# Kernel tuning notes

Measured on AMD Instinct MI355X. Metric: run time of the kernel, lower is better.

Reference implementation:

```python
import jax, jax.numpy as jnp
import numpy as np

D_MODEL = 1024
H = 16
D_K = D_MODEL // H
NEG = -1e9


def setup_inputs() -> dict:
    key = jax.random.key(0)
    ks = jax.random.split(key, 13)
    B, S = 4, 2048
    q = jax.random.normal(ks[0], (B, S, D_MODEL), dtype=jnp.float32)
    k = jax.random.normal(ks[1], (B, S, D_MODEL), dtype=jnp.float32)
    v = jax.random.normal(ks[2], (B, S, D_MODEL), dtype=jnp.float32)
    mask = jax.random.randint(ks[3], (B, 1, S, S), 0, 2, dtype=jnp.int32)
    s = 1.0 / np.sqrt(D_MODEL)
    wq = jax.random.uniform(ks[4], (D_MODEL, D_MODEL), jnp.float32, -s, s)
    bq = jax.random.uniform(ks[5], (D_MODEL,), jnp.float32, -s, s)
    wk = jax.random.uniform(ks[6], (D_MODEL, D_MODEL), jnp.float32, -s, s)
    bk = jax.random.uniform(ks[7], (D_MODEL,), jnp.float32, -s, s)
    wv = jax.random.uniform(ks[8], (D_MODEL, D_MODEL), jnp.float32, -s, s)
    bv = jax.random.uniform(ks[9], (D_MODEL,), jnp.float32, -s, s)
    wo = jax.random.uniform(ks[10], (D_MODEL, D_MODEL), jnp.float32, -s, s)
    bo = jax.random.uniform(ks[11], (D_MODEL,), jnp.float32, -s, s)
    return {"q": q, "k": k, "v": v, "mask": mask,
            "wq": wq, "bq": bq, "wk": wk, "bk": bk,
            "wv": wv, "bv": bv, "wo": wo, "bo": bo}


def reference(q, k, v, mask, wq, bq, wk, bk, wv, bv, wo, bo):
    B, S, _ = q.shape
    # projections (torch Linear: x @ W.T + b)
    query = q @ wq.T + bq
    key_ = k @ wk.T + bk
    value = v @ wv.T + bv
    # [B, S, H, D_K] -> [B, H, S, D_K]
    query = query.reshape(B, S, H, D_K).transpose(0, 2, 1, 3)
    key_ = key_.reshape(B, S, H, D_K).transpose(0, 2, 1, 3)
    value = value.reshape(B, S, H, D_K).transpose(0, 2, 1, 3)
    scores = jnp.einsum('bhqd,bhkd->bhqk', query, key_) / jnp.sqrt(jnp.float32(D_K))
    scores = jnp.where(mask == 0, jnp.float32(NEG), scores)
    attn = jax.nn.softmax(scores, axis=-1)  # dropout p=0 -> identity
    x = jnp.einsum('bhqk,bhkd->bhqd', attn, value)
    x = x.transpose(0, 2, 1, 3).reshape(B, S, D_MODEL)
    return x @ wo.T + bo
```

## Files before the change

### kernel.cpp

```cpp
#include <hip/hip_runtime.h>
#include <stdint.h>
#include <stddef.h>


typedef unsigned short ushort_t;
typedef unsigned long long u64;
typedef __attribute__((ext_vector_type(8))) short short8;
typedef __attribute__((ext_vector_type(4))) float floatx4;
typedef __attribute__((ext_vector_type(4))) unsigned short ushort4v;
typedef __attribute__((ext_vector_type(4))) unsigned int uint4v;

#define QSCALE (0.125f * 1.4426950408889634f)

__device__ __forceinline__ ushort_t f2bf(float f) {
    union { float ff; unsigned int i; } v; v.ff = f;
    unsigned int u = v.i;
    return (ushort_t)((u + 0x7fffu + ((u >> 16) & 1u)) >> 16);
}
__device__ __forceinline__ unsigned int pk2(float a, float b) {
    unsigned int r;
    asm("v_cvt_pk_bf16_f32 %0, %1, %2" : "=v"(r) : "v"(a), "v"(b));
    return r;
}
__device__ __forceinline__ float fexp2(float x) {
#if __has_builtin(__builtin_amdgcn_exp2f)
    return __builtin_amdgcn_exp2f(x);
#else
    return exp2f(x);
#endif
}
__device__ __forceinline__ void g2l16(const void* g, void* l) {
    __builtin_amdgcn_global_load_lds(
        (const __attribute__((address_space(1))) void*)(uintptr_t)g,
        (__attribute__((address_space(3))) void*)(uint32_t)(uintptr_t)l,
        16, 0, 0);
}
__device__ __forceinline__ void cvt_store(ushort_t* d0, ushort_t* d1,
        float4 a, float4 b, float4 c, float4 d) {
    uint4v c0, c1;
    c0.x = pk2(a.x, a.y); c0.y = pk2(a.z, a.w);
    c0.z = pk2(b.x, b.y); c0.w = pk2(b.z, b.w);
    c1.x = pk2(c.x, c.y); c1.y = pk2(c.z, c.w);
    c1.z = pk2(d.x, d.y); c1.w = pk2(d.z, d.w);
    *(uint4v*)d0 = c0;
    *(uint4v*)d1 = c1;
}

__global__ __launch_bounds__(256) void prep(
    const float* __restrict__ wq, const float* __restrict__ wk,
    const float* __restrict__ wv, const float* __restrict__ wo,
    const int* __restrict__ mask,
    ushort_t* __restrict__ Wb, u64* __restrict__ mbits)
{
    const int bx = blockIdx.x, tid = threadIdx.x;
    if (bx < 2048) {
        const int seg = bx >> 9;
        const float* src = (seg == 0) ? wq : (seg == 1) ? wk
                         : (seg == 2) ? wv : wo;
        ushort_t* dst = Wb + (size_t)seg * 1024 * 1024;
        const int idx = (bx & 511) * 256 + tid;
        const float4 f0 = ((const float4*)src)[idx * 2];
        const float4 f1 = ((const float4*)src)[idx * 2 + 1];
        uint4v c;
        c.x = pk2(f0.x, f0.y); c.y = pk2(f0.z, f0.w);
        c.z = pk2(f1.x, f1.y); c.w = pk2(f1.z, f1.w);
        ((uint4v*)dst)[idx] = c;
    } else {
        const int b3 = bx - 2048;
        const int base = b3 * 4096;
#pragma unroll
        for (int it = 0; it < 16; ++it) {
            const int gid = base + it * 256 + tid;
            const u64 bits = __ballot(mask[gid] != 0);
            if ((tid & 63) == 0) mbits[gid >> 6] = bits;
        }
    }
}

__device__ __forceinline__ void gemm_epilogue(
    floatx4 (&acc)[4][4], const float* __restrict__ bias,
    void* __restrict__ Cout, float scale, int mode,
    int bm, int bn, int wm, int wn, int quad, int l16)
{
    constexpr int N = 1024;
#pragma unroll
    for (int ni = 0; ni < 4; ni++) {
        const int n = bn + wn * 64 + ni * 16 + l16;
        const float bv_ = bias[n];
#pragma unroll
        for (int mi = 0; mi < 4; mi++) {
            const int mbase = bm + wm * 64 + mi * 16 + quad * 4;
            if (mode == 2) {
                const int b_ = mbase >> 11, s0 = mbase & 2047;
                const int h = n >> 6, d = n & 63;
                ushort4v pk_;
#pragma unroll
                for (int r = 0; r < 4; r++)
                    pk_[r] = f2bf((acc[mi][ni][r] + bv_) * scale);
                *(ushort4v*)&((ushort_t*)Cout)[
                    (((size_t)(b_ * 16 + h)) * 64 + d) * 2048 + s0] = pk_;
            } else {
#pragma unroll
                for (int r = 0; r < 4; r++) {
                    const int m = mbase + r;
                    const float of = (acc[mi][ni][r] + bv_) * scale;
                    if (mode == 0) {
                        ((float*)Cout)[(size_t)m * N + n] = of;
                    } else {
                        const int b_ = m >> 11, s = m & 2047;
                        const int h = n >> 6, d = n & 63;
                        ((ushort_t*)Cout)[(((size_t)(b_ * 16 + h)) * 2048 + s) * 64 + d]
                            = f2bf(of);
                    }
                }
            }
        }
    }
}

__device__ __forceinline__ void gemm_core_f32(
    const float* __restrict__ Ain, const ushort_t* __restrict__ W,
    const float* __restrict__ bias, void* __restrict__ Cout,
    float scale, int mode)
{
    constexpr int K = 1024;
    __shared__ alignas(16) ushort_t As[2][128 * 32];
    __shared__ alignas(16) ushort_t Bs[2][128 * 32];

    const int tid  = threadIdx.x;
    const int lane = tid & 63;
    const int w    = tid >> 6;
    const int quad = lane >> 4;
    const int l16  = lane & 15;
    const int wm = w >> 1, wn = w & 1;
    const int bm = blockIdx.x * 128, bn = blockIdx.y * 128;

    const int wrow = tid >> 2;
    const int wcs  = ((tid & 3) ^ ((tid >> 3) & 3)) * 8;
    const ushort_t* Wst0 = W + (size_t)(bn + wrow) * K + wcs;
    const ushort_t* Wst1 = W + (size_t)(bn + wrow + 64) * K + wcs;

    const int arow = tid >> 1, ahalf = tid & 1;
    const float* Af = Ain + (size_t)(bm + arow) * K + ahalf * 16;
    const int fa  = (tid >> 2) & 3;
    const int ac0 = ((2 * ahalf + 0) ^ fa) * 8;
    const int ac1 = ((2 * ahalf + 1) ^ fa) * 8;

    const int ksw = (quad ^ ((l16 >> 1) & 3)) * 8;
    int asoff[4], bsoff[4];
#pragma unroll
    for (int i = 0; i < 4; i++) {
        asoff[i] = (wm * 64 + i * 16 + l16) * 32 + ksw;
        bsoff[i] = (wn * 64 + i * 16 + l16) * 32 + ksw;
    }

    floatx4 acc[4][4] = {};

    {
        const float4* ap = (const float4*)Af;
        const float4 f0 = ap[0], f1 = ap[1], f2 = ap[2], f3 = ap[3];
        g2l16(Wst0, &Bs[0][tid * 8]);
        g2l16(Wst1, &Bs[0][(tid + 256) * 8]);
        cvt_store(&As[0][arow * 32 + ac0], &As[0][arow * 32 + ac1],
                  f0, f1, f2, f3);
    }
    __syncthreads();

    int cur = 0;
    for (int kt = 0; kt < K; kt += 32) {
        const int nxt = kt + 32;
        float4 f0, f1, f2, f3;
        if (nxt < K) {
            const float4* ap = (const float4*)(Af + nxt);
            f0 = ap[0]; f1 = ap[1]; f2 = ap[2]; f3 = ap[3];
            g2l16(Wst0 + nxt, &Bs[cur ^ 1][tid * 8]);
            g2l16(Wst1 + nxt, &Bs[cur ^ 1][(tid + 256) * 8]);
        }

        short8 af[4], bf[4];
#pragma unroll
        for (int i = 0; i < 4; i++) af[i] = *(const short8*)&As[cur][asoff[i]];
#pragma unroll
        for (int i = 0; i < 4; i++) bf[i] = *(const short8*)&Bs[cur][bsoff[i]];
        __builtin_amdgcn_s_setprio(1);
#pragma unroll
        for (int mi = 0; mi < 4; mi++)
#pragma unroll
            for (int ni = 0; ni < 4; ni++)
                acc[mi][ni] = __builtin_amdgcn_mfma_f32_16x16x32_bf16(
                    af[mi], bf[ni], acc[mi][ni], 0, 0, 0);
        __builtin_amdgcn_s_setprio(0);

        if (nxt < K)
            cvt_store(&As[cur ^ 1][arow * 32 + ac0],
                      &As[cur ^ 1][arow * 32 + ac1], f0, f1, f2, f3);
        __syncthreads();
        cur ^= 1;
    }

    gemm_epilogue(acc, bias, Cout, scale, mode, bm, bn, wm, wn, quad, l16);
}

__device__ __forceinline__ void gemm_core_bf16(
    const ushort_t* __restrict__ Ain, const ushort_t* __restrict__ W,
    const float* __restrict__ bias, void* __restrict__ Cout,
    float scale, int mode)
{
    constexpr int K = 1024;
    __shared__ alignas(16) ushort_t As[4][128 * 32];
    __shared__ alignas(16) ushort_t Bs[2][128 * 32];

    const int tid  = threadIdx.x;
    const int lane = tid & 63;
    const int w    = tid >> 6;
    const int quad = lane >> 4;
    const int l16  = lane & 15;
    const int wm = w >> 1, wn = w & 1;
    const int bm = blockIdx.x * 128, bn = blockIdx.y * 128;

    const int srow = tid >> 2;
    const int scs  = ((tid & 3) ^ ((tid >> 3) & 3)) * 8;
    const ushort_t* Ast0 = Ain + (size_t)(bm + srow) * K + scs;
    const ushort_t* Ast1 = Ain + (size_t)(bm + srow + 64) * K + scs;
    const ushort_t* Wst0 = W + (size_t)(bn + srow) * K + scs;
    const ushort_t* Wst1 = W + (size_t)(bn + srow + 64) * K + scs;

    const int ksw = (quad ^ ((l16 >> 1) & 3)) * 8;
    int asoff[4], bsoff[4];
#pragma unroll
    for (int i = 0; i < 4; i++) {
        asoff[i] = (wm * 64 + i * 16 + l16) * 32 + ksw;
        bsoff[i] = (wn * 64 + i * 16 + l16) * 32 + ksw;
    }

    floatx4 acc[4][4] = {};

    g2l16(Wst0,      &Bs[0][tid * 8]);
    g2l16(Wst1,      &Bs[0][(tid + 256) * 8]);
    __builtin_amdgcn_sched_barrier(0);
    g2l16(Ast0,      &As[0][tid * 8]);
    g2l16(Ast1,      &As[0][(tid + 256) * 8]);
    g2l16(Ast0 + 32, &As[1][tid * 8]);
    g2l16(Ast1 + 32, &As[1][(tid + 256) * 8]);
    g2l16(Ast0 + 64, &As[2][tid * 8]);
    g2l16(Ast1 + 64, &As[2][(tid + 256) * 8]);

#define GITER(AS, WS, NW, NA, KW, KA, DO_W, DO_A, TOPW) do {                  \
    asm volatile("s_waitcnt " TOPW);                                          \
    asm volatile("s_waitcnt lgkmcnt(0)");                                     \
    __builtin_amdgcn_sched_barrier(0);                                        \
    __builtin_amdgcn_s_barrier();                                             \
    __builtin_amdgcn_sched_barrier(0);                                        \
    if (DO_W) {                                                               \
        g2l16(Wst0 + (KW), &Bs[NW][tid * 8]);                                 \
        g2l16(Wst1 + (KW), &Bs[NW][(tid + 256) * 8]);                         \
    }                                                                         \
    __builtin_amdgcn_sched_barrier(0);                                        \
    if (DO_A) {                                                               \
        g2l16(Ast0 + (KA), &As[NA][tid * 8]);                                 \
        g2l16(Ast1 + (KA), &As[NA][(tid + 256) * 8]);                         \
    }                                                                         \
    __builtin_amdgcn_sched_barrier(0);                                        \
    {                                                                         \
        short8 af[4], bf[4];                                                  \
        _Pragma("unroll")                                                     \
        for (int i = 0; i < 4; i++) af[i] = *(const short8*)&As[AS][asoff[i]];\
        _Pragma("unroll")                                                     \
        for (int i = 0; i < 4; i++) bf[i] = *(const short8*)&Bs[WS][bsoff[i]];\
        __builtin_amdgcn_s_setprio(1);                                        \
        _Pragma("unroll")                                                     \
        for (int mi = 0; mi < 4; mi++)                                        \
        _Pragma("unroll")                                                     \
        for (int ni = 0; ni < 4; ni++)                                        \
            acc[mi][ni] = __builtin_amdgcn_mfma_f32_16x16x32_bf16(            \
                af[mi], bf[ni], acc[mi][ni], 0, 0, 0);                        \
        __builtin_amdgcn_s_setprio(0);                                        \
    }                                                                         \
} while (0)

    GITER(0, 0, 1, 3,  32,  96, true, true, "vmcnt(4)");
    GITER(1, 1, 0, 0,  64, 128, true, true, "vmcnt(2)");
    GITER(2, 0, 1, 1,  96, 160, true, true, "vmcnt(2)");
    GITER(3, 1, 0, 2, 128, 192, true, true, "vmcnt(2)");
    for (int j = 1; j < 7; ++j) {
        const int kb = j * 128;
        GITER(0, 0, 1, 3, kb + 32,  kb + 96,  true, true, "vmcnt(2)");
        GITER(1, 1, 0, 0, kb + 64,  kb + 128, true, true, "vmcnt(2)");
        GITER(2, 0, 1, 1, kb + 96,  kb + 160, true, true, "vmcnt(2)");
        GITER(3, 1, 0, 2, kb + 128, kb + 192, true, true, "vmcnt(2)");
    }
    GITER(0, 0, 1, 3, 928, 992, true,  true,  "vmcnt(2)");
    GITER(1, 1, 0, 0, 960, 0,   true,  false, "vmcnt(2)");
    GITER(2, 0, 1, 0, 992, 0,   true,  false, "vmcnt(0)");
    GITER(3, 1, 0, 0, 0,   0,   false, false, "vmcnt(0)");
#undef GITER

    gemm_epilogue(acc, bias, Cout, scale, mode, bm, bn, wm, wn, quad, l16);
}

__global__ __launch_bounds__(256, 2) void gemm_qkv(
    const float* __restrict__ q, const float* __restrict__ k,
    const float* __restrict__ v, const ushort_t* __restrict__ Wb,
    const float* __restrict__ bq, const float* __restrict__ bk,
    const float* __restrict__ bv,
    ushort_t* __restrict__ Qp, ushort_t* __restrict__ Kp,
    ushort_t* __restrict__ Vtp)
{
    const int z = blockIdx.z;
    const float* A = (z == 0) ? q : (z == 1) ? k : v;
    const ushort_t* W = Wb + (size_t)z * 1024 * 1024;
    const float* bi = (z == 0) ? bq : (z == 1) ? bk : bv;
    void* C = (z == 0) ? (void*)Qp : (z == 1) ? (void*)Kp : (void*)Vtp;
    const float sc = (z == 0) ? QSCALE : 1.0f;
    const int mode = (z == 2) ? 2 : 1;
    gemm_core_f32(A, W, bi, C, sc, mode);
}

__global__ __launch_bounds__(256, 3) void gemm_out(
    const ushort_t* __restrict__ X, const ushort_t* __restrict__ W,
    const float* __restrict__ bo, float* __restrict__ out)
{
    gemm_core_bf16(X, W, bo, out, 1.0f, 0);
}

__global__ __launch_bounds__(256, 4) void attn(
    const ushort_t* __restrict__ Q,
    const ushort_t* __restrict__ Kk,
    const ushort_t* __restrict__ Vt,
    const u64* __restrict__ mb,
    ushort_t* __restrict__ X)
{
    constexpr int S = 2048;
    __shared__ alignas(16) ushort_t Ks[2][64 * 64];
    __shared__ alignas(16) ushort_t Vs[2][64 * 64];
    __shared__ alignas(16) ushort_t Ps[4][16 * 64];

    const int tid  = threadIdx.x;
    const int lane = tid & 63;
    const int w    = tid >> 6;
    const int quad = lane >> 4;
    const int l16  = lane & 15;
    const int bh = blockIdx.x;
    const int b  = bh >> 4, h = bh & 15;
    const int qbase = blockIdx.y * 64 + w * 16;
    const int qlane = qbase + l16;

    const int r0 = tid >> 3,         cs0 = ((tid & 7) ^ (r0 & 7)) * 8;
    const int r1 = (tid + 256) >> 3, cs1 = ((tid & 7) ^ (r1 & 7)) * 8;

    const ushort_t* Kst0 = &Kk[((size_t)bh * S + r0) * 64 + cs0];
    const ushort_t* Kst1 = &Kk[((size_t)bh * S + r1) * 64 + cs1];
    const ushort_t* Vst0 = &Vt[((size_t)bh * 64 + r0) * S + cs0];
    const ushort_t* Vst1 = &Vt[((size_t)bh * 64 + r1) * S + cs1];

    const int swz = l16 & 7;
    int kvoff[2][4], pfoff[2], pwoff[4];
#pragma unroll
    for (int ks = 0; ks < 2; ks++) {
        pfoff[ks] = l16 * 64 + (((ks * 4 + quad) ^ swz) * 8);
#pragma unroll
        for (int ni = 0; ni < 4; ni++)
            kvoff[ks][ni] = (ni * 16 + l16) * 64 + (((ks * 4 + quad) ^ swz) * 8);
    }
#pragma unroll
    for (int ni = 0; ni < 4; ni++)
        pwoff[ni] = l16 * 64 + (((ni * 2 + (quad >> 1)) ^ swz) * 8) + (quad & 1) * 4;
    ushort_t* Psw = &Ps[w][0];

    short8 qf[2];
#pragma unroll
    for (int ks = 0; ks < 2; ks++)
        qf[ks] = *(const short8*)&Q[((size_t)bh * S + qlane) * 64 + ks * 32 + quad * 8];

    short8 onesv;
#pragma unroll
    for (int i = 0; i < 8; i++) onesv[i] = (short)0x3F80;

    const u64* mrow = mb + ((size_t)b * S + qlane) * 32;

    floatx4 o[4] = {};
    floatx4 lf = {};

    g2l16(Kst0, &Ks[0][tid * 8]);
    g2l16(Kst1, &Ks[0][(tid + 256) * 8]);
    g2l16(Vst0, &Vs[0][tid * 8]);
    g2l16(Vst1, &Vs[0][(tid + 256) * 8]);
    __syncthreads();

    u64 mw = mrow[0];
    int cur = 0;
    for (int kt = 0; kt < 32; kt++) {
        u64 mw_nxt = 0;
        if (kt < 31) {
            mw_nxt = mrow[kt + 1];
            g2l16(Kst0 + (kt + 1) * 4096, &Ks[cur ^ 1][tid * 8]);
            g2l16(Kst1 + (kt + 1) * 4096, &Ks[cur ^ 1][(tid + 256) * 8]);
            g2l16(Vst0 + (kt + 1) * 64,   &Vs[cur ^ 1][tid * 8]);
            g2l16(Vst1 + (kt + 1) * 64,   &Vs[cur ^ 1][(tid + 256) * 8]);
        }
        const ushort_t* Ksc = &Ks[cur][0];
        const ushort_t* Vsc = &Vs[cur][0];

        floatx4 s[4] = {};
        __builtin_amdgcn_s_setprio(1);
#pragma unroll
        for (int ks = 0; ks < 2; ks++)
#pragma unroll
            for (int ni = 0; ni < 4; ni++)
                s[ni] = __builtin_amdgcn_mfma_f32_16x16x32_bf16(
                    *(const short8*)&Ksc[kvoff[ks][ni]], qf[ks], s[ni], 0, 0, 0);
        __builtin_amdgcn_s_setprio(0);

#pragma unroll
        for (int ni = 0; ni < 4; ni++) {
            const unsigned int t = (unsigned int)(mw >> (ni * 16 + quad * 4));
#pragma unroll
            for (int r = 0; r < 4; r++)
                s[ni][r] = (t & (1u << r)) ? fexp2(s[ni][r]) : 0.f;
        }

#pragma unroll
        for (int ni = 0; ni < 4; ni++) {
            const unsigned int lo = pk2(s[ni][0], s[ni][1]);
            const unsigned int hi = pk2(s[ni][2], s[ni][3]);
            const unsigned long long dv = ((unsigned long long)hi << 32) | lo;
            *(unsigned long long*)&Psw[pwoff[ni]] = dv;
        }

        __builtin_amdgcn_s_setprio(1);
#pragma unroll
        for (int ks = 0; ks < 2; ks++) {
            const short8 pf = *(const short8*)&Psw[pfoff[ks]];
            lf = __builtin_amdgcn_mfma_f32_16x16x32_bf16(onesv, pf, lf, 0, 0, 0);
#pragma unroll
            for (int ni = 0; ni < 4; ni++)
                o[ni] = __builtin_amdgcn_mfma_f32_16x16x32_bf16(
                    *(const short8*)&Vsc[kvoff[ks][ni]], pf, o[ni], 0, 0, 0);
        }
        __builtin_amdgcn_s_setprio(0);
        __syncthreads();
        mw = mw_nxt;
        cur ^= 1;
    }

    const float inv = 1.0f / lf[0];
#pragma unroll
    for (int ni = 0; ni < 4; ni++) {
        ushort4v pk_;
#pragma unroll
        for (int r = 0; r < 4; r++) pk_[r] = f2bf(o[ni][r] * inv);
        *(ushort4v*)&X[((size_t)b * S + qlane) * 1024 + h * 64 + ni * 16 + quad * 4] = pk_;
    }
}

extern "C" void kernel_launch(void* const* d_in, const int* in_sizes, int n_in,
                              void* d_out, int out_size, void* d_ws, size_t ws_size,
                              hipStream_t stream) {
    const float* q    = (const float*)d_in[0];
    const float* k    = (const float*)d_in[1];
    const float* v    = (const float*)d_in[2];
    const int*   mask = (const int*)d_in[3];
    const float* wq   = (const float*)d_in[4];
    const float* bq   = (const float*)d_in[5];
    const float* wk   = (const float*)d_in[6];
    const float* bk   = (const float*)d_in[7];
    const float* wv   = (const float*)d_in[8];
    const float* bv   = (const float*)d_in[9];
    const float* wo   = (const float*)d_in[10];
    const float* bo   = (const float*)d_in[11];

    const size_t MB = 1024 * 1024;
    uint8_t* ws = (uint8_t*)d_ws;
    ushort_t* Wb   = (ushort_t*)(ws);
    u64*      mbits= (u64*)(ws + 8 * MB);
    ushort_t* Qp   = (ushort_t*)(ws + 10 * MB);
    ushort_t* Kp   = (ushort_t*)(ws + 26 * MB);
    ushort_t* Vtp  = (ushort_t*)(ws + 42 * MB);
    ushort_t* Xp   = (ushort_t*)(ws + 58 * MB);

    dim3 blk(256);

    prep<<<dim3(6144), blk, 0, stream>>>(wq, wk, wv, wo, mask, Wb, mbits);

    gemm_qkv<<<dim3(64, 8, 3), blk, 0, stream>>>(q, k, v, Wb, bq, bk, bv,
                                                 Qp, Kp, Vtp);

    attn<<<dim3(64, 32), blk, 0, stream>>>(Qp, Kp, Vtp, mbits, Xp);

    gemm_out<<<dim3(64, 8), blk, 0, stream>>>(Xp, Wb + 3 * MB, bo, (float*)d_out);
}
```

Baseline: 427.0 us.

## Shrink output GEMM tile to 64x128, raise occupancy, drop setprio

```diff
diff --git a/kernel.cpp b/kernel.cpp
--- a/kernel.cpp
+++ b/kernel.cpp
@@ -82,7 +82,6 @@
     void* __restrict__ Cout, float scale, int mode,
     int bm, int bn, int wm, int wn, int quad, int l16)
 {
-    constexpr int N = 1024;
 #pragma unroll
     for (int ni = 0; ni < 4; ni++) {
         const int n = bn + wn * 64 + ni * 16 + l16;
@@ -104,14 +103,10 @@
                 for (int r = 0; r < 4; r++) {
                     const int m = mbase + r;
                     const float of = (acc[mi][ni][r] + bv_) * scale;
-                    if (mode == 0) {
-                        ((float*)Cout)[(size_t)m * N + n] = of;
-                    } else {
-                        const int b_ = m >> 11, s = m & 2047;
-                        const int h = n >> 6, d = n & 63;
-                        ((ushort_t*)Cout)[(((size_t)(b_ * 16 + h)) * 2048 + s) * 64 + d]
-                            = f2bf(of);
-                    }
+                    const int b_ = m >> 11, s = m & 2047;
+                    const int h = n >> 6, d = n & 63;
+                    ((ushort_t*)Cout)[(((size_t)(b_ * 16 + h)) * 2048 + s) * 64 + d]
+                        = f2bf(of);
                 }
             }
         }
@@ -182,14 +177,12 @@
         for (int i = 0; i < 4; i++) af[i] = *(const short8*)&As[cur][asoff[i]];
 #pragma unroll
         for (int i = 0; i < 4; i++) bf[i] = *(const short8*)&Bs[cur][bsoff[i]];
-        __builtin_amdgcn_s_setprio(1);
 #pragma unroll
         for (int mi = 0; mi < 4; mi++)
 #pragma unroll
             for (int ni = 0; ni < 4; ni++)
                 acc[mi][ni] = __builtin_amdgcn_mfma_f32_16x16x32_bf16(
                     af[mi], bf[ni], acc[mi][ni], 0, 0, 0);
-        __builtin_amdgcn_s_setprio(0);
 
         if (nxt < K)
             cvt_store(&As[cur ^ 1][arow * 32 + ac0],
@@ -201,13 +194,30 @@
     gemm_epilogue(acc, bias, Cout, scale, mode, bm, bn, wm, wn, quad, l16);
 }
 
-__device__ __forceinline__ void gemm_core_bf16(
+__global__ __launch_bounds__(256, 3) void gemm_qkv(
+    const float* __restrict__ q, const float* __restrict__ k,
+    const float* __restrict__ v, const ushort_t* __restrict__ Wb,
+    const float* __restrict__ bq, const float* __restrict__ bk,
+    const float* __restrict__ bv,
+    ushort_t* __restrict__ Qp, ushort_t* __restrict__ Kp,
+    ushort_t* __restrict__ Vtp)
+{
+    const int z = blockIdx.z;
+    const float* A = (z == 0) ? q : (z == 1) ? k : v;
+    const ushort_t* W = Wb + (size_t)z * 1024 * 1024;
+    const float* bi = (z == 0) ? bq : (z == 1) ? bk : bv;
+    void* C = (z == 0) ? (void*)Qp : (z == 1) ? (void*)Kp : (void*)Vtp;
+    const float sc = (z == 0) ? QSCALE : 1.0f;
+    const int mode = (z == 2) ? 2 : 1;
+    gemm_core_f32(A, W, bi, C, sc, mode);
+}
+
+__global__ __launch_bounds__(256, 4) void gemm_out(
     const ushort_t* __restrict__ Ain, const ushort_t* __restrict__ W,
-    const float* __restrict__ bias, void* __restrict__ Cout,
-    float scale, int mode)
-{
-    constexpr int K = 1024;
-    __shared__ alignas(16) ushort_t As[4][128 * 32];
+    const float* __restrict__ bias, float* __restrict__ out)
+{
+    constexpr int K = 1024, N = 1024;
+    __shared__ alignas(16) ushort_t As[4][64 * 32];
     __shared__ alignas(16) ushort_t Bs[2][128 * 32];
 
     const int tid  = threadIdx.x;
@@ -216,36 +226,33 @@
     const int quad = lane >> 4;
     const int l16  = lane & 15;
     const int wm = w >> 1, wn = w & 1;
-    const int bm = blockIdx.x * 128, bn = blockIdx.y * 128;
+    const int bm = blockIdx.x * 64, bn = blockIdx.y * 128;
 
     const int srow = tid >> 2;
     const int scs  = ((tid & 3) ^ ((tid >> 3) & 3)) * 8;
-    const ushort_t* Ast0 = Ain + (size_t)(bm + srow) * K + scs;
-    const ushort_t* Ast1 = Ain + (size_t)(bm + srow + 64) * K + scs;
+    const ushort_t* Ast  = Ain + (size_t)(bm + srow) * K + scs;
     const ushort_t* Wst0 = W + (size_t)(bn + srow) * K + scs;
     const ushort_t* Wst1 = W + (size_t)(bn + srow + 64) * K + scs;
 
     const int ksw = (quad ^ ((l16 >> 1) & 3)) * 8;
-    int asoff[4], bsoff[4];
-#pragma unroll
-    for (int i = 0; i < 4; i++) {
-        asoff[i] = (wm * 64 + i * 16 + l16) * 32 + ksw;
+    int asoff[2], bsoff[4];
+#pragma unroll
+    for (int i = 0; i < 2; i++)
+        asoff[i] = (wm * 32 + i * 16 + l16) * 32 + ksw;
+#pragma unroll
+    for (int i = 0; i < 4; i++)
         bsoff[i] = (wn * 64 + i * 16 + l16) * 32 + ksw;
-    }
-
-    floatx4 acc[4][4] = {};
+
+    floatx4 acc[2][4] = {};
 
     g2l16(Wst0,      &Bs[0][tid * 8]);
     g2l16(Wst1,      &Bs[0][(tid + 256) * 8]);
     __builtin_amdgcn_sched_barrier(0);
-    g2l16(Ast0,      &As[0][tid * 8]);
-    g2l16(Ast1,      &As[0][(tid + 256) * 8]);
-    g2l16(Ast0 + 32, &As[1][tid * 8]);
-    g2l16(Ast1 + 32, &As[1][(tid + 256) * 8]);
-    g2l16(Ast0 + 64, &As[2][tid * 8]);
-    g2l16(Ast1 + 64, &As[2][(tid + 256) * 8]);
-
-#define GITER(AS, WS, NW, NA, KW, KA, DO_W, DO_A, TOPW) do {                  \
+    g2l16(Ast,       &As[0][tid * 8]);
+    g2l16(Ast + 32,  &As[1][tid * 8]);
+    g2l16(Ast + 64,  &As[2][tid * 8]);
+
+#define OITER(AS, WS, NW, NA, KW, KA, DO_W, DO_A, TOPW) do {                  \
     asm volatile("s_waitcnt " TOPW);                                          \
     asm volatile("s_waitcnt lgkmcnt(0)");                                     \
     __builtin_amdgcn_sched_barrier(0);                                        \
@@ -256,71 +263,52 @@
         g2l16(Wst1 + (KW), &Bs[NW][(tid + 256) * 8]);                         \
     }                                                                         \
     __builtin_amdgcn_sched_barrier(0);                                        \
-    if (DO_A) {                                                               \
-        g2l16(Ast0 + (KA), &As[NA][tid * 8]);                                 \
-        g2l16(Ast1 + (KA), &As[NA][(tid + 256) * 8]);                         \
-    }                                                                         \
+    if (DO_A) g2l16(Ast + (KA), &As[NA][tid * 8]);                            \
     __builtin_amdgcn_sched_barrier(0);                                        \
     {                                                                         \
-        short8 af[4], bf[4];                                                  \
+        short8 af[2], bf[4];                                                  \
         _Pragma("unroll")                                                     \
-        for (int i = 0; i < 4; i++) af[i] = *(const short8*)&As[AS][asoff[i]];\
+        for (int i = 0; i < 2; i++) af[i] = *(const short8*)&As[AS][asoff[i]];\
         _Pragma("unroll")                                                     \
         for (int i = 0; i < 4; i++) bf[i] = *(const short8*)&Bs[WS][bsoff[i]];\
-        __builtin_amdgcn_s_setprio(1);                                        \
         _Pragma("unroll")                                                     \
-        for (int mi = 0; mi < 4; mi++)                                        \
+        for (int mi = 0; mi < 2; mi++)                                        \
         _Pragma("unroll")                                                     \
         for (int ni = 0; ni < 4; ni++)                                        \
             acc[mi][ni] = __builtin_amdgcn_mfma_f32_16x16x32_bf16(            \
                 af[mi], bf[ni], acc[mi][ni], 0, 0, 0);                        \
-        __builtin_amdgcn_s_setprio(0);                                        \
     }                                                                         \
 } while (0)
 
-    GITER(0, 0, 1, 3,  32,  96, true, true, "vmcnt(4)");
-    GITER(1, 1, 0, 0,  64, 128, true, true, "vmcnt(2)");
-    GITER(2, 0, 1, 1,  96, 160, true, true, "vmcnt(2)");
-    GITER(3, 1, 0, 2, 128, 192, true, true, "vmcnt(2)");
+    OITER(0, 0, 1, 3,  32,  96, true, true, "vmcnt(2)");
+    OITER(1, 1, 0, 0,  64, 128, true, true, "vmcnt(1)");
+    OITER(2, 0, 1, 1,  96, 160, true, true, "vmcnt(1)");
+    OITER(3, 1, 0, 2, 128, 192, true, true, "vmcnt(1)");
     for (int j = 1; j < 7; ++j) {
         const int kb = j * 128;
-        GITER(0, 0, 1, 3, kb + 32,  kb + 96,  true, true, "vmcnt(2)");
-        GITER(1, 1, 0, 0, kb + 64,  kb + 128, true, true, "vmcnt(2)");
-        GITER(2, 0, 1, 1, kb + 96,  kb + 160, true, true, "vmcnt(2)");
-        GITER(3, 1, 0, 2, kb + 128, kb + 192, true, true, "vmcnt(2)");
-    }
-    GITER(0, 0, 1, 3, 928, 992, true,  true,  "vmcnt(2)");
-    GITER(1, 1, 0, 0, 960, 0,   true,  false, "vmcnt(2)");
-    GITER(2, 0, 1, 0, 992, 0,   true,  false, "vmcnt(0)");
-    GITER(3, 1, 0, 0, 0,   0,   false, false, "vmcnt(0)");
-#undef GITER
-
-    gemm_epilogue(acc, bias, Cout, scale, mode, bm, bn, wm, wn, quad, l16);
-}
-
-__global__ __launch_bounds__(256, 2) void gemm_qkv(
-    const float* __restrict__ q, const float* __restrict__ k,
-    const float* __restrict__ v, const ushort_t* __restrict__ Wb,
-    const float* __restrict__ bq, const float* __restrict__ bk,
-    const float* __restrict__ bv,
-    ushort_t* __restrict__ Qp, ushort_t* __restrict__ Kp,
-    ushort_t* __restrict__ Vtp)
-{
-    const int z = blockIdx.z;
-    const float* A = (z == 0) ? q : (z == 1) ? k : v;
-    const ushort_t* W = Wb + (size_t)z * 1024 * 1024;
-    const float* bi = (z == 0) ? bq : (z == 1) ? bk : bv;
-    void* C = (z == 0) ? (void*)Qp : (z == 1) ? (void*)Kp : (void*)Vtp;
-    const float sc = (z == 0) ? QSCALE : 1.0f;
-    const int mode = (z == 2) ? 2 : 1;
-    gemm_core_f32(A, W, bi, C, sc, mode);
-}
-
-__global__ __launch_bounds__(256, 3) void gemm_out(
-    const ushort_t* __restrict__ X, const ushort_t* __restrict__ W,
-    const float* __restrict__ bo, float* __restrict__ out)
-{
-    gemm_core_bf16(X, W, bo, out, 1.0f, 0);
+        OITER(0, 0, 1, 3, kb + 32,  kb + 96,  true, true, "vmcnt(1)");
+        OITER(1, 1, 0, 0, kb + 64,  kb + 128, true, true, "vmcnt(1)");
+        OITER(2, 0, 1, 1, kb + 96,  kb + 160, true, true, "vmcnt(1)");
+        OITER(3, 1, 0, 2, kb + 128, kb + 192, true, true, "vmcnt(1)");
+    }
+    OITER(0, 0, 1, 3, 928, 992, true,  true,  "vmcnt(1)");
+    OITER(1, 1, 0, 0, 960, 0,   true,  false, "vmcnt(1)");
+    OITER(2, 0, 1, 0, 992, 0,   true,  false, "vmcnt(0)");
+    OITER(3, 1, 0, 0, 0,   0,   false, false, "vmcnt(0)");
+#undef OITER
+
+#pragma unroll
+    for (int ni = 0; ni < 4; ni++) {
+        const int n = bn + wn * 64 + ni * 16 + l16;
+        const float bv_ = bias[n];
+#pragma unroll
+        for (int mi = 0; mi < 2; mi++) {
+            const int mbase = bm + wm * 32 + mi * 16 + quad * 4;
+#pragma unroll
+            for (int r = 0; r < 4; r++)
+                out[(size_t)(mbase + r) * N + n] = acc[mi][ni][r] + bv_;
+        }
+    }
 }
 
 __global__ __launch_bounds__(256, 4) void attn(
@@ -487,5 +475,5 @@
 
     attn<<<dim3(64, 32), blk, 0, stream>>>(Qp, Kp, Vtp, mbits, Xp);
 
-    gemm_out<<<dim3(64, 8), blk, 0, stream>>>(Xp, Wb + 3 * MB, bo, (float*)d_out);
-}
+    gemm_out<<<dim3(128, 8), blk, 0, stream>>>(Xp, Wb + 3 * MB, bo, (float*)d_out);
+}
```

Measured after the change: 428.0 us. No clear change (+0.2%).

## Deepen f32-A prefetch in QKV GEMM with unrolled manual-waitcnt pipeline

Applied to the files above, without the earlier changes.

```diff
diff --git a/kernel.cpp b/kernel.cpp
--- a/kernel.cpp
+++ b/kernel.cpp
@@ -155,48 +155,67 @@
     }
 
     floatx4 acc[4][4] = {};
+    float4 fA[4], fB[4];
 
     {
-        const float4* ap = (const float4*)Af;
-        const float4 f0 = ap[0], f1 = ap[1], f2 = ap[2], f3 = ap[3];
+        const float4* a0 = (const float4*)Af;
+        fA[0] = a0[0]; fA[1] = a0[1]; fA[2] = a0[2]; fA[3] = a0[3];
+        const float4* a1 = (const float4*)(Af + 32);
+        fB[0] = a1[0]; fB[1] = a1[1]; fB[2] = a1[2]; fB[3] = a1[3];
         g2l16(Wst0, &Bs[0][tid * 8]);
         g2l16(Wst1, &Bs[0][(tid + 256) * 8]);
         cvt_store(&As[0][arow * 32 + ac0], &As[0][arow * 32 + ac1],
-                  f0, f1, f2, f3);
+                  fA[0], fA[1], fA[2], fA[3]);
     }
     __syncthreads();
 
-    int cur = 0;
-    for (int kt = 0; kt < K; kt += 32) {
-        const int nxt = kt + 32;
-        float4 f0, f1, f2, f3;
-        if (nxt < K) {
-            const float4* ap = (const float4*)(Af + nxt);
-            f0 = ap[0]; f1 = ap[1]; f2 = ap[2]; f3 = ap[3];
-            g2l16(Wst0 + nxt, &Bs[cur ^ 1][tid * 8]);
-            g2l16(Wst1 + nxt, &Bs[cur ^ 1][(tid + 256) * 8]);
-        }
-
-        short8 af[4], bf[4];
-#pragma unroll
-        for (int i = 0; i < 4; i++) af[i] = *(const short8*)&As[cur][asoff[i]];
-#pragma unroll
-        for (int i = 0; i < 4; i++) bf[i] = *(const short8*)&Bs[cur][bsoff[i]];
-        __builtin_amdgcn_s_setprio(1);
-#pragma unroll
-        for (int mi = 0; mi < 4; mi++)
-#pragma unroll
-            for (int ni = 0; ni < 4; ni++)
-                acc[mi][ni] = __builtin_amdgcn_mfma_f32_16x16x32_bf16(
-                    af[mi], bf[ni], acc[mi][ni], 0, 0, 0);
-        __builtin_amdgcn_s_setprio(0);
-
-        if (nxt < K)
-            cvt_store(&As[cur ^ 1][arow * 32 + ac0],
-                      &As[cur ^ 1][arow * 32 + ac1], f0, f1, f2, f3);
-        __syncthreads();
-        cur ^= 1;
-    }
+#define FITER(CUR, FST, FLD, WOFF, AOFF, DO_W, DO_A, DO_C, VM) do {           \
+    if (DO_W) {                                                               \
+        g2l16(Wst0 + (WOFF), &Bs[(CUR) ^ 1][tid * 8]);                        \
+        g2l16(Wst1 + (WOFF), &Bs[(CUR) ^ 1][(tid + 256) * 8]);                \
+    }                                                                         \
+    __builtin_amdgcn_sched_barrier(0);                                        \
+    if (DO_A) {                                                               \
+        const float4* ap_ = (const float4*)(Af + (AOFF));                     \
+        FLD[0] = ap_[0]; FLD[1] = ap_[1]; FLD[2] = ap_[2]; FLD[3] = ap_[3];   \
+    }                                                                         \
+    __builtin_amdgcn_sched_barrier(0);                                        \
+    {                                                                         \
+        short8 af_[4], bf_[4];                                                \
+        _Pragma("unroll")                                                     \
+        for (int i = 0; i < 4; i++)                                           \
+            af_[i] = *(const short8*)&As[CUR][asoff[i]];                      \
+        _Pragma("unroll")                                                     \
+        for (int i = 0; i < 4; i++)                                           \
+            bf_[i] = *(const short8*)&Bs[CUR][bsoff[i]];                      \
+        _Pragma("unroll")                                                     \
+        for (int mi = 0; mi < 4; mi++)                                        \
+        _Pragma("unroll")                                                     \
+        for (int ni = 0; ni < 4; ni++)                                        \
+            acc[mi][ni] = __builtin_amdgcn_mfma_f32_16x16x32_bf16(            \
+                af_[mi], bf_[ni], acc[mi][ni], 0, 0, 0);                      \
+    }                                                                         \
+    if (DO_C)                                                                 \
+        cvt_store(&As[(CUR) ^ 1][arow * 32 + ac0],                            \
+                  &As[(CUR) ^ 1][arow * 32 + ac1],                            \
+                  FST[0], FST[1], FST[2], FST[3]);                            \
+    asm volatile("s_waitcnt " VM);                                            \
+    asm volatile("s_waitcnt lgkmcnt(0)");                                     \
+    __builtin_amdgcn_sched_barrier(0);                                        \
+    __builtin_amdgcn_s_barrier();                                             \
+    __builtin_amdgcn_sched_barrier(0);                                        \
+} while (0)
+
+    for (int j = 0; j < 14; ++j) {
+        const int t = 2 * j;
+        FITER(0, fB, fA, (t + 1) * 32, (t + 2) * 32, true, true, true, "vmcnt(4)");
+        FITER(1, fA, fB, (t + 2) * 32, (t + 3) * 32, true, true, true, "vmcnt(4)");
+    }
+    FITER(0, fB, fA, 29 * 32, 30 * 32, true,  true,  true,  "vmcnt(4)");
+    FITER(1, fA, fB, 30 * 32, 31 * 32, true,  true,  true,  "vmcnt(4)");
+    FITER(0, fB, fA, 31 * 32, 0,       true,  false, true,  "vmcnt(0)");
+    FITER(1, fA, fB, 0,       0,       false, false, false, "vmcnt(0)");
+#undef FITER
 
     gemm_epilogue(acc, bias, Cout, scale, mode, bm, bn, wm, wn, quad, l16);
 }
@@ -258,7 +277,7 @@
     __builtin_amdgcn_sched_barrier(0);                                        \
     if (DO_A) {                                                               \
         g2l16(Ast0 + (KA), &As[NA][tid * 8]);                                 \
-        g2l16(Ast1 + (KA), &As[NA][(tid + 256) * 8]);                         \
+        g2l16(Ast1 + (KA), &As[NA][(tid + 256) * 8]);                        \
     }                                                                         \
     __builtin_amdgcn_sched_barrier(0);                                        \
     {                                                                         \
@@ -267,14 +286,12 @@
         for (int i = 0; i < 4; i++) af[i] = *(const short8*)&As[AS][asoff[i]];\
         _Pragma("unroll")                                                     \
         for (int i = 0; i < 4; i++) bf[i] = *(const short8*)&Bs[WS][bsoff[i]];\
-        __builtin_amdgcn_s_setprio(1);                                        \
         _Pragma("unroll")                                                     \
         for (int mi = 0; mi < 4; mi++)                                        \
         _Pragma("unroll")                                                     \
         for (int ni = 0; ni < 4; ni++)                                        \
             acc[mi][ni] = __builtin_amdgcn_mfma_f32_16x16x32_bf16(            \
                 af[mi], bf[ni], acc[mi][ni], 0, 0, 0);                        \
-        __builtin_amdgcn_s_setprio(0);                                        \
     }                                                                         \
 } while (0)
 
@@ -298,7 +315,7 @@
     gemm_epilogue(acc, bias, Cout, scale, mode, bm, bn, wm, wn, quad, l16);
 }
 
-__global__ __launch_bounds__(256, 2) void gemm_qkv(
+__global__ __launch_bounds__(256, 3) void gemm_qkv(
     const float* __restrict__ q, const float* __restrict__ k,
     const float* __restrict__ v, const ushort_t* __restrict__ Wb,
     const float* __restrict__ bq, const float* __restrict__ bk,
```

New measurement: 427.1 us. Within noise of the previous version (+0.0%).
